# Optimization experiments

Measured on AMD Instinct MI355X. Metric: run time of the kernel, lower is better.

## Reference

```python
import jax, jax.numpy as jnp
import numpy as np

V, E, H, B, S = 50000, 256, 256, 64, 2048


def setup_inputs() -> dict:
    key = jax.random.key(0)
    ks = jax.random.split(key, 13)
    u = lambda k, shape: jax.random.uniform(k, shape, jnp.float32) - 0.5
    return {
        "inp": jax.random.randint(ks[0], (B,), 0, V, dtype=jnp.int64),
        "hidden": jax.random.normal(ks[1], (1, B, H), jnp.float32),
        "encoder_outputs": jax.random.normal(ks[2], (B, S, H), jnp.float32),
        "emb": jax.random.normal(ks[3], (V, E), jnp.float32),          # nn.Embedding weight
        "U": u(ks[4], (H, H)),
        "W": u(ks[5], (H, H)),
        "v": u(ks[6], (H, 1)),
        "W_ih": u(ks[7], (H, E)),   # RNN weight_ih_l0
        "W_hh": u(ks[8], (H, H)),   # RNN weight_hh_l0
        "b_ih": u(ks[9], (H,)),
        "b_hh": u(ks[10], (H,)),
        "W_out": u(ks[11], (V, H)),  # output Linear weight
        "b_out": u(ks[12], (V,)),
    }


def reference(inp, hidden, encoder_outputs, emb, U, W, v,
              W_ih, W_hh, b_ih, b_hh, W_out, b_out):
    # embedding lookup: (B, E)
    x = emb[inp]
    word_embs = x[:, None, :]                         # (B, 1, E)
    # Bahdanau additive attention (get_context)
    summed = jnp.tanh(word_embs @ U + encoder_outputs @ W)   # (B, S, H)
    e_ij = summed @ v                                        # (B, S, 1)
    alpha = jax.nn.softmax(e_ij, axis=1)                     # (B, S, 1)
    context = jnp.sum(alpha * encoder_outputs, axis=1)       # (B, H)
    # single tanh-RNN step; NOTE: original code feeds context as initial hidden,
    # ignoring the `hidden` argument when attention is enabled.
    h_new = jnp.tanh(x @ W_ih.T + b_ih + context @ W_hh.T + b_hh)  # (B, H)
    logits = h_new @ W_out.T + b_out                               # (B, V)
    return logits, h_new[None]                                     # hidden: (1, B, H)
```

## Files before the change

### kernel.cpp

```cpp
#include <hip/hip_runtime.h>
#include <hip/hip_bf16.h>
#include <math.h>

#define V_ 50000
#define E_ 256
#define H_ 256
#define B_ 64
#define S_ 2048
#define NCHK 32

typedef __attribute__((ext_vector_type(4))) float f32x4;
typedef __attribute__((ext_vector_type(8))) __bf16 bf16x8;

static __device__ __forceinline__ f32x4 mfma16(bf16x8 a, bf16x8 b, f32x4 c) {
  return __builtin_amdgcn_mfma_f32_16x16x32_bf16(a, b, c, 0, 0, 0);
}
static __device__ __forceinline__ float fast_tanh(float x) {
  const float e2 = __expf(2.0f * x);
  return 1.0f - 2.0f / (e2 + 1.0f);
}

__global__ __launch_bounds__(256) void prep_k(
    const int* __restrict__ inp, const float* __restrict__ emb,
    const float* __restrict__ U, const float* __restrict__ W_ih,
    const float* __restrict__ b_ih, const float* __restrict__ b_hh,
    float* __restrict__ xU, float* __restrict__ xWih) {
  const int b = blockIdx.x, h = threadIdx.x;
  __shared__ float xs[H_];
  xs[h] = emb[(size_t)inp[b] * E_ + h];
  __syncthreads();
  float au = 0.f, aw = 0.f;
  const float* __restrict__ wir = W_ih + (size_t)h * E_;
  for (int k = 0; k < H_; k += 4) {
    const float4 x4 = *reinterpret_cast<const float4*>(&xs[k]);
    const float4 w4 = *reinterpret_cast<const float4*>(wir + k);
    aw = fmaf(x4.x, w4.x, aw); aw = fmaf(x4.y, w4.y, aw);
    aw = fmaf(x4.z, w4.z, aw); aw = fmaf(x4.w, w4.w, aw);
    au = fmaf(x4.x, U[(size_t)(k + 0) * H_ + h], au);
    au = fmaf(x4.y, U[(size_t)(k + 1) * H_ + h], au);
    au = fmaf(x4.z, U[(size_t)(k + 2) * H_ + h], au);
    au = fmaf(x4.w, U[(size_t)(k + 3) * H_ + h], au);
  }
  xU[b * H_ + h] = au;
  xWih[b * H_ + h] = aw + b_ih[h] + b_hh[h];
}

__global__ __launch_bounds__(256) void prep_w(
    const float* __restrict__ W, __bf16* __restrict__ wt) {
  const int idx = blockIdx.x * 256 + threadIdx.x;
  const int n = idx >> 8, k = idx & 255;
  wt[n * H_ + (k ^ ((n & 7) << 3))] = (__bf16)W[(size_t)k * H_ + n];
}

__global__ __launch_bounds__(512) void attn_fused(
    const float* __restrict__ enc, const __bf16* __restrict__ wt,
    const float* __restrict__ xU, const float* __restrict__ vv,
    float* __restrict__ ctxp, float* __restrict__ mlout) {
  const int bx = blockIdx.x, b = blockIdx.y;
  const int t = threadIdx.x;
  const int w = t >> 6, l = t & 63, l15 = l & 15, lg = l >> 4;
  const int rg = w >> 1, cg = w & 1;

  __shared__ __bf16 Wl[H_ * H_];
  __shared__ float ered[2][128];
  __shared__ float wgt[128];
  __shared__ float mlL[2][2];

  {
    const bf16x8* __restrict__ src = reinterpret_cast<const bf16x8*>(wt);
    bf16x8* dst = reinterpret_cast<bf16x8*>(Wl);
#pragma unroll
    for (int i = 0; i < 16; ++i) dst[i * 512 + t] = src[i * 512 + t];
  }
  __syncthreads();

  for (int si = 0; si < 2; ++si) {
    const int s0 = (bx * 2 + si) * 128;
    const float* __restrict__ encS = enc + ((size_t)b * S_ + s0) * H_;
    const float* __restrict__ a0 = encS + (size_t)(rg * 32 + l15) * H_ + lg * 8;
    const float* __restrict__ a1 = encS + (size_t)(rg * 32 + 16 + l15) * H_ + lg * 8;

    f32x4 acc[2][8];
#pragma unroll
    for (int rf = 0; rf < 2; ++rf)
#pragma unroll
      for (int cf = 0; cf < 8; ++cf) acc[rf][cf] = (f32x4)(0.f);

    float4 af[2][2][2];
    af[0][0][0] = *reinterpret_cast<const float4*>(a0);
    af[0][0][1] = *reinterpret_cast<const float4*>(a0 + 4);
    af[0][1][0] = *reinterpret_cast<const float4*>(a1);
    af[0][1][1] = *reinterpret_cast<const float4*>(a1 + 4);

#pragma unroll
    for (int k = 0; k < 8; ++k) {
      const int cb = k & 1;
      if (k < 7) {
        af[cb ^ 1][0][0] = *reinterpret_cast<const float4*>(a0 + (k + 1) * 32);
        af[cb ^ 1][0][1] = *reinterpret_cast<const float4*>(a0 + (k + 1) * 32 + 4);
        af[cb ^ 1][1][0] = *reinterpret_cast<const float4*>(a1 + (k + 1) * 32);
        af[cb ^ 1][1][1] = *reinterpret_cast<const float4*>(a1 + (k + 1) * 32 + 4);
      }
      bf16x8 bb[8];
#pragma unroll
      for (int cf = 0; cf < 8; ++cf) {
        const int col = cg * 128 + cf * 16 + l15;
        bb[cf] = *reinterpret_cast<const bf16x8*>(
            &Wl[col * H_ + ((k * 32 + lg * 8) ^ ((col & 7) << 3))]);
      }
      bf16x8 ahi[2], alo[2];
#pragma unroll
      for (int rf = 0; rf < 2; ++rf) {
        const float xa[8] = {af[cb][rf][0].x, af[cb][rf][0].y, af[cb][rf][0].z, af[cb][rf][0].w,
                             af[cb][rf][1].x, af[cb][rf][1].y, af[cb][rf][1].z, af[cb][rf][1].w};
#pragma unroll
        for (int j = 0; j < 8; ++j) {
          const __bf16 hh = (__bf16)xa[j];
          ahi[rf][j] = hh;
          alo[rf][j] = (__bf16)(xa[j] - (float)hh);
        }
      }
#pragma unroll
      for (int rf = 0; rf < 2; ++rf)
#pragma unroll
        for (int cf = 0; cf < 8; ++cf) {
          acc[rf][cf] = mfma16(ahi[rf], bb[cf], acc[rf][cf]);
          acc[rf][cf] = mfma16(alo[rf], bb[cf], acc[rf][cf]);
        }
    }

    float part[2][4];
#pragma unroll
    for (int rf = 0; rf < 2; ++rf)
#pragma unroll
      for (int reg = 0; reg < 4; ++reg) part[rf][reg] = 0.f;
#pragma unroll
    for (int cf = 0; cf < 8; ++cf) {
      const int col = cg * 128 + cf * 16 + l15;
      const float xu = xU[b * H_ + col];
      const float vw = vv[col];
#pragma unroll
      for (int rf = 0; rf < 2; ++rf)
#pragma unroll
        for (int reg = 0; reg < 4; ++reg)
          part[rf][reg] += fast_tanh(xu + acc[rf][cf][reg]) * vw;
    }
#pragma unroll
    for (int o = 1; o < 16; o <<= 1)
#pragma unroll
      for (int rf = 0; rf < 2; ++rf)
#pragma unroll
        for (int reg = 0; reg < 4; ++reg)
          part[rf][reg] += __shfl_xor(part[rf][reg], o);
    if (l15 == 0) {
#pragma unroll
      for (int rf = 0; rf < 2; ++rf)
#pragma unroll
        for (int reg = 0; reg < 4; ++reg)
          ered[cg][rg * 32 + rf * 16 + lg * 4 + reg] = part[rf][reg];
    }
    __syncthreads();

    if (t < 128) {
      const float es = ered[0][t] + ered[1][t];
      float m = es;
#pragma unroll
      for (int o = 1; o < 64; o <<= 1) m = fmaxf(m, __shfl_xor(m, o));
      const float we = __expf(es - m);
      float ls = we;
#pragma unroll
      for (int o = 1; o < 64; o <<= 1) ls += __shfl_xor(ls, o);
      wgt[t] = we;
      if ((t & 63) == 0) { mlL[t >> 6][0] = m; mlL[t >> 6][1] = ls; }
    }
    __syncthreads();

    {
      const int c2 = t >> 8, h = t & 255;
      const float* __restrict__ ep = encS + (size_t)(c2 * 64) * H_ + h;
      float a = 0.f;
#pragma unroll 8
      for (int s = 0; s < 64; ++s) a = fmaf(wgt[c2 * 64 + s], ep[(size_t)s * H_], a);
      ctxp[((size_t)(bx * 4 + si * 2 + c2) * B_ + b) * H_ + h] = a;
    }
    if ((t & 255) == 0) {
      const int c2 = t >> 8;
      mlout[((bx * 4 + si * 2 + c2) * B_ + b) * 2 + 0] = mlL[c2][0];
      mlout[((bx * 4 + si * 2 + c2) * B_ + b) * 2 + 1] = mlL[c2][1];
    }
    __syncthreads();
  }
}

__global__ __launch_bounds__(256) void combine_hnew(
    const float* __restrict__ ctxp, const float* __restrict__ mlout,
    const float* __restrict__ xWih, const float* __restrict__ W_hh,
    float* __restrict__ out_h, __bf16* __restrict__ hn) {
  const int b = blockIdx.x, h = threadIdx.x;
  __shared__ float cs[H_];
  float M = -3.4e38f;
#pragma unroll
  for (int cc = 0; cc < NCHK; ++cc) M = fmaxf(M, mlout[(cc * B_ + b) * 2]);
  float num = 0.f, den = 0.f;
#pragma unroll
  for (int cc = 0; cc < NCHK; ++cc) {
    const float mw = __expf(mlout[(cc * B_ + b) * 2] - M);
    den = fmaf(mw, mlout[(cc * B_ + b) * 2 + 1], den);
    num = fmaf(mw, ctxp[((size_t)cc * B_ + b) * H_ + h], num);
  }
  cs[h] = num / den;
  __syncthreads();
  const float* __restrict__ wr = W_hh + (size_t)h * H_;
  float a = xWih[b * H_ + h];
  for (int k = 0; k < H_; k += 4) {
    const float4 w4 = *reinterpret_cast<const float4*>(wr + k);
    const float4 c4 = *reinterpret_cast<const float4*>(&cs[k]);
    a = fmaf(c4.x, w4.x, a); a = fmaf(c4.y, w4.y, a);
    a = fmaf(c4.z, w4.z, a); a = fmaf(c4.w, w4.w, a);
  }
  const float hv = fast_tanh(a);
  out_h[b * H_ + h] = hv;
  hn[b * H_ + h] = (__bf16)hv;
}

__global__ __launch_bounds__(256) void logits_mfma(
    const float* __restrict__ Wout, const float* __restrict__ bout,
    const __bf16* __restrict__ hn, float* __restrict__ logits) {
  const int v0 = blockIdx.x * 64;
  const int t = threadIdx.x;
  const int wv = t >> 6, l = t & 63, l15 = l & 15, lg = l >> 4;

  __shared__ __bf16 Wsub[8][64][32];

  {
    const int srow = t >> 2, sg = t & 3;
    const int wslot = (sg + (srow >> 1)) & 3;
    const int vc = (v0 + srow) < V_ ? (v0 + srow) : (V_ - 1);
    const float* __restrict__ wr = Wout + (size_t)vc * H_ + sg * 8;
#pragma unroll
    for (int ks = 0; ks < 8; ++ks) {
      const float4 f0 = *reinterpret_cast<const float4*>(wr + ks * 32);
      const float4 f1 = *reinterpret_cast<const float4*>(wr + ks * 32 + 4);
      const float xv[8] = {f0.x, f0.y, f0.z, f0.w, f1.x, f1.y, f1.z, f1.w};
      bf16x8 h8;
#pragma unroll
      for (int j = 0; j < 8; ++j) h8[j] = (__bf16)xv[j];
      *reinterpret_cast<bf16x8*>(&Wsub[ks][srow][wslot * 8]) = h8;
    }
  }
  __syncthreads();

  f32x4 acc[4];
#pragma unroll
  for (int i = 0; i < 4; ++i) acc[i] = (f32x4)(0.f);
  const int colb = wv * 16 + l15;
#pragma unroll
  for (int k = 0; k < 8; ++k) {
    const bf16x8 bfrag = *reinterpret_cast<const bf16x8*>(hn + (size_t)colb * H_ + k * 32 + lg * 8);
    bf16x8 ah[4];
#pragma unroll
    for (int rf = 0; rf < 4; ++rf) {
      const int rr = rf * 16 + l15;
      const int slot = (lg + (rr >> 1)) & 3;
      ah[rf] = *reinterpret_cast<const bf16x8*>(&Wsub[k][rr][slot * 8]);
    }
#pragma unroll
    for (int rf = 0; rf < 4; ++rf)
      acc[rf] = mfma16(ah[rf], bfrag, acc[rf]);
  }
#pragma unroll
  for (int rf = 0; rf < 4; ++rf) {
    const int v = v0 + rf * 16 + lg * 4;
    if (v < V_) {
      const float4 bo = *reinterpret_cast<const float4*>(bout + v);
      float4 o;
      o.x = acc[rf][0] + bo.x; o.y = acc[rf][1] + bo.y;
      o.z = acc[rf][2] + bo.z; o.w = acc[rf][3] + bo.w;
      *reinterpret_cast<float4*>(logits + (size_t)colb * V_ + v) = o;
    }
  }
}

extern "C" void kernel_launch(void* const* d_in, const int* in_sizes, int n_in,
                              void* d_out, int out_size, void* d_ws, size_t ws_size,
                              hipStream_t stream) {
  const int*   inp  = (const int*)  d_in[0];
  const float* enc  = (const float*)d_in[2];
  const float* emb  = (const float*)d_in[3];
  const float* U    = (const float*)d_in[4];
  const float* W    = (const float*)d_in[5];
  const float* v    = (const float*)d_in[6];
  const float* W_ih = (const float*)d_in[7];
  const float* W_hh = (const float*)d_in[8];
  const float* b_ih = (const float*)d_in[9];
  const float* b_hh = (const float*)d_in[10];
  const float* Wout = (const float*)d_in[11];
  const float* bout = (const float*)d_in[12];

  float* logits = (float*)d_out;
  float* out_h  = logits + (size_t)B_ * V_;

  float* ws    = (float*)d_ws;
  __bf16* wt   = (__bf16*)ws;
  float* xU    = ws + 32768;
  float* xWih  = xU + B_ * H_;
  float* ctxp  = xWih + B_ * H_;
  float* mlout = ctxp + (size_t)NCHK * B_ * H_;
  __bf16* hn   = (__bf16*)(mlout + NCHK * B_ * 2);

  prep_k<<<dim3(B_), dim3(256), 0, stream>>>(inp, emb, U, W_ih, b_ih, b_hh, xU, xWih);
  prep_w<<<dim3(H_ * H_ / 256), dim3(256), 0, stream>>>(W, wt);
  attn_fused<<<dim3(8, B_), dim3(512), 0, stream>>>(enc, wt, xU, v, ctxp, mlout);
  combine_hnew<<<dim3(B_), dim3(256), 0, stream>>>(ctxp, mlout, xWih, W_hh, out_h, hn);
  logits_mfma<<<dim3((V_ + 63) / 64), dim3(256), 0, stream>>>(Wout, bout, hn, logits);
}
```

Baseline: 111.0 us.

## Switch attention GEMM to 32x32x16 MFMA with k-octet W layout and 256-row units

```diff
diff --git a/kernel.cpp b/kernel.cpp
--- a/kernel.cpp
+++ b/kernel.cpp
@@ -10,10 +10,14 @@
 #define NCHK 32
 
 typedef __attribute__((ext_vector_type(4))) float f32x4;
+typedef __attribute__((ext_vector_type(16))) float f32x16;
 typedef __attribute__((ext_vector_type(8))) __bf16 bf16x8;
 
 static __device__ __forceinline__ f32x4 mfma16(bf16x8 a, bf16x8 b, f32x4 c) {
   return __builtin_amdgcn_mfma_f32_16x16x32_bf16(a, b, c, 0, 0, 0);
+}
+static __device__ __forceinline__ f32x16 mfma32(bf16x8 a, bf16x8 b, f32x16 c) {
+  return __builtin_amdgcn_mfma_f32_32x32x16_bf16(a, b, c, 0, 0, 0);
 }
 static __device__ __forceinline__ float fast_tanh(float x) {
   const float e2 = __expf(2.0f * x);
@@ -46,123 +50,111 @@
 }
 
 __global__ __launch_bounds__(256) void prep_w(
-    const float* __restrict__ W, __bf16* __restrict__ wt) {
+    const float* __restrict__ W, __bf16* __restrict__ wt2) {
   const int idx = blockIdx.x * 256 + threadIdx.x;
-  const int n = idx >> 8, k = idx & 255;
-  wt[n * H_ + (k ^ ((n & 7) << 3))] = (__bf16)W[(size_t)k * H_ + n];
-}
-
-__global__ __launch_bounds__(512) void attn_fused(
-    const float* __restrict__ enc, const __bf16* __restrict__ wt,
+  const int k = idx >> 8, col = idx & 255;
+  wt2[((size_t)(k >> 3) * 256 + col) * 8 + (k & 7)] = (__bf16)W[(size_t)k * H_ + col];
+}
+
+__global__ __launch_bounds__(512, 2) void attn_fused(
+    const float* __restrict__ enc, const __bf16* __restrict__ wt2,
     const float* __restrict__ xU, const float* __restrict__ vv,
     float* __restrict__ ctxp, float* __restrict__ mlout) {
-  const int bx = blockIdx.x, b = blockIdx.y;
   const int t = threadIdx.x;
-  const int w = t >> 6, l = t & 63, l15 = l & 15, lg = l >> 4;
-  const int rg = w >> 1, cg = w & 1;
-
-  __shared__ __bf16 Wl[H_ * H_];
-  __shared__ float ered[2][128];
-  __shared__ float wgt[128];
-  __shared__ float mlL[2][2];
+  const int w = t >> 6, l = t & 63, l31 = l & 31, h5 = l >> 5;
+
+  __shared__ __bf16 Wl[32 * 256 * 8];
+  __shared__ float ered[256];
+  __shared__ float wgt[4][64];
+  __shared__ float mlL[4][2];
 
   {
-    const bf16x8* __restrict__ src = reinterpret_cast<const bf16x8*>(wt);
+    const bf16x8* __restrict__ src = reinterpret_cast<const bf16x8*>(wt2);
     bf16x8* dst = reinterpret_cast<bf16x8*>(Wl);
 #pragma unroll
     for (int i = 0; i < 16; ++i) dst[i * 512 + t] = src[i * 512 + t];
   }
+  float xu[8], vw[8];
   __syncthreads();
 
-  for (int si = 0; si < 2; ++si) {
-    const int s0 = (bx * 2 + si) * 128;
-    const float* __restrict__ encS = enc + ((size_t)b * S_ + s0) * H_;
-    const float* __restrict__ a0 = encS + (size_t)(rg * 32 + l15) * H_ + lg * 8;
-    const float* __restrict__ a1 = encS + (size_t)(rg * 32 + 16 + l15) * H_ + lg * 8;
-
-    f32x4 acc[2][8];
-#pragma unroll
-    for (int rf = 0; rf < 2; ++rf)
-#pragma unroll
-      for (int cf = 0; cf < 8; ++cf) acc[rf][cf] = (f32x4)(0.f);
-
-    float4 af[2][2][2];
-    af[0][0][0] = *reinterpret_cast<const float4*>(a0);
-    af[0][0][1] = *reinterpret_cast<const float4*>(a0 + 4);
-    af[0][1][0] = *reinterpret_cast<const float4*>(a1);
-    af[0][1][1] = *reinterpret_cast<const float4*>(a1 + 4);
-
-#pragma unroll
-    for (int k = 0; k < 8; ++k) {
-      const int cb = k & 1;
-      if (k < 7) {
-        af[cb ^ 1][0][0] = *reinterpret_cast<const float4*>(a0 + (k + 1) * 32);
-        af[cb ^ 1][0][1] = *reinterpret_cast<const float4*>(a0 + (k + 1) * 32 + 4);
-        af[cb ^ 1][1][0] = *reinterpret_cast<const float4*>(a1 + (k + 1) * 32);
-        af[cb ^ 1][1][1] = *reinterpret_cast<const float4*>(a1 + (k + 1) * 32 + 4);
+#pragma unroll 1
+  for (int uu = 0; uu < 2; ++uu) {
+    const int unit = blockIdx.x * 2 + uu;
+    const int b = unit >> 3;
+    const int sidx = unit & 7;
+    const int s0 = sidx * 256;
+
+    const float* __restrict__ encA =
+        enc + ((size_t)b * S_ + s0 + w * 32 + l31) * H_ + h5 * 8;
+
+    f32x16 acc[8];
+#pragma unroll
+    for (int cf = 0; cf < 8; ++cf) acc[cf] = (f32x16)(0.f);
+
+    float4 af[2][2];
+    af[0][0] = *reinterpret_cast<const float4*>(encA);
+    af[0][1] = *reinterpret_cast<const float4*>(encA + 4);
+
+#pragma unroll
+    for (int ks = 0; ks < 16; ++ks) {
+      const int cb = ks & 1;
+      if (ks < 15) {
+        af[cb ^ 1][0] = *reinterpret_cast<const float4*>(encA + (ks + 1) * 16);
+        af[cb ^ 1][1] = *reinterpret_cast<const float4*>(encA + (ks + 1) * 16 + 4);
       }
       bf16x8 bb[8];
-#pragma unroll
-      for (int cf = 0; cf < 8; ++cf) {
-        const int col = cg * 128 + cf * 16 + l15;
+      const int koct = ks * 2 + h5;
+#pragma unroll
+      for (int cf = 0; cf < 8; ++cf)
         bb[cf] = *reinterpret_cast<const bf16x8*>(
-            &Wl[col * H_ + ((k * 32 + lg * 8) ^ ((col & 7) << 3))]);
-      }
-      bf16x8 ahi[2], alo[2];
-#pragma unroll
-      for (int rf = 0; rf < 2; ++rf) {
-        const float xa[8] = {af[cb][rf][0].x, af[cb][rf][0].y, af[cb][rf][0].z, af[cb][rf][0].w,
-                             af[cb][rf][1].x, af[cb][rf][1].y, af[cb][rf][1].z, af[cb][rf][1].w};
+            &Wl[((size_t)koct * 256 + cf * 32 + l31) * 8]);
+      bf16x8 ahi, alo;
+      {
+        const float xa[8] = {af[cb][0].x, af[cb][0].y, af[cb][0].z, af[cb][0].w,
+                             af[cb][1].x, af[cb][1].y, af[cb][1].z, af[cb][1].w};
 #pragma unroll
         for (int j = 0; j < 8; ++j) {
           const __bf16 hh = (__bf16)xa[j];
-          ahi[rf][j] = hh;
-          alo[rf][j] = (__bf16)(xa[j] - (float)hh);
+          ahi[j] = hh;
+          alo[j] = (__bf16)(xa[j] - (float)hh);
         }
       }
 #pragma unroll
-      for (int rf = 0; rf < 2; ++rf)
-#pragma unroll
-        for (int cf = 0; cf < 8; ++cf) {
-          acc[rf][cf] = mfma16(ahi[rf], bb[cf], acc[rf][cf]);
-          acc[rf][cf] = mfma16(alo[rf], bb[cf], acc[rf][cf]);
-        }
-    }
-
-    float part[2][4];
-#pragma unroll
-    for (int rf = 0; rf < 2; ++rf)
-#pragma unroll
-      for (int reg = 0; reg < 4; ++reg) part[rf][reg] = 0.f;
+      for (int cf = 0; cf < 8; ++cf) acc[cf] = mfma32(ahi, bb[cf], acc[cf]);
+#pragma unroll
+      for (int cf = 0; cf < 8; ++cf) acc[cf] = mfma32(alo, bb[cf], acc[cf]);
+    }
+
 #pragma unroll
     for (int cf = 0; cf < 8; ++cf) {
-      const int col = cg * 128 + cf * 16 + l15;
-      const float xu = xU[b * H_ + col];
-      const float vw = vv[col];
-#pragma unroll
-      for (int rf = 0; rf < 2; ++rf)
-#pragma unroll
-        for (int reg = 0; reg < 4; ++reg)
-          part[rf][reg] += fast_tanh(xu + acc[rf][cf][reg]) * vw;
-    }
-#pragma unroll
-    for (int o = 1; o < 16; o <<= 1)
-#pragma unroll
-      for (int rf = 0; rf < 2; ++rf)
-#pragma unroll
-        for (int reg = 0; reg < 4; ++reg)
-          part[rf][reg] += __shfl_xor(part[rf][reg], o);
-    if (l15 == 0) {
-#pragma unroll
-      for (int rf = 0; rf < 2; ++rf)
-#pragma unroll
-        for (int reg = 0; reg < 4; ++reg)
-          ered[cg][rg * 32 + rf * 16 + lg * 4 + reg] = part[rf][reg];
+      const int col = cf * 32 + l31;
+      xu[cf] = xU[b * H_ + col];
+      vw[cf] = vv[col];
+    }
+    float rs[16];
+#pragma unroll
+    for (int reg = 0; reg < 16; ++reg) {
+      float s = 0.f;
+#pragma unroll
+      for (int cf = 0; cf < 8; ++cf)
+        s += fast_tanh(xu[cf] + acc[cf][reg]) * vw[cf];
+      rs[reg] = s;
+    }
+#pragma unroll
+    for (int o = 1; o < 32; o <<= 1)
+#pragma unroll
+      for (int reg = 0; reg < 16; ++reg)
+        rs[reg] += __shfl_xor(rs[reg], o);
+    if (l31 == 0) {
+#pragma unroll
+      for (int reg = 0; reg < 16; ++reg)
+        ered[w * 32 + (reg & 3) + 8 * (reg >> 2) + 4 * h5] = rs[reg];
     }
     __syncthreads();
 
-    if (t < 128) {
-      const float es = ered[0][t] + ered[1][t];
+    if (t < 256) {
+      const int cidx = t >> 6, rr = t & 63;
+      const float es = ered[cidx * 64 + rr];
       float m = es;
 #pragma unroll
       for (int o = 1; o < 64; o <<= 1) m = fmaxf(m, __shfl_xor(m, o));
@@ -170,23 +162,24 @@
       float ls = we;
 #pragma unroll
       for (int o = 1; o < 64; o <<= 1) ls += __shfl_xor(ls, o);
-      wgt[t] = we;
-      if ((t & 63) == 0) { mlL[t >> 6][0] = m; mlL[t >> 6][1] = ls; }
+      wgt[cidx][rr] = we;
+      if (rr == 0) { mlL[cidx][0] = m; mlL[cidx][1] = ls; }
     }
     __syncthreads();
 
-    {
-      const int c2 = t >> 8, h = t & 255;
-      const float* __restrict__ ep = encS + (size_t)(c2 * 64) * H_ + h;
+#pragma unroll
+    for (int it = 0; it < 2; ++it) {
+      const int cc = (t >> 8) + it * 2;
+      const int h = t & 255;
+      const float* __restrict__ ep = enc + ((size_t)b * S_ + s0 + cc * 64) * H_ + h;
       float a = 0.f;
 #pragma unroll 8
-      for (int s = 0; s < 64; ++s) a = fmaf(wgt[c2 * 64 + s], ep[(size_t)s * H_], a);
-      ctxp[((size_t)(bx * 4 + si * 2 + c2) * B_ + b) * H_ + h] = a;
-    }
-    if ((t & 255) == 0) {
-      const int c2 = t >> 8;
-      mlout[((bx * 4 + si * 2 + c2) * B_ + b) * 2 + 0] = mlL[c2][0];
-      mlout[((bx * 4 + si * 2 + c2) * B_ + b) * 2 + 1] = mlL[c2][1];
+      for (int s = 0; s < 64; ++s) a = fmaf(wgt[cc][s], ep[(size_t)s * H_], a);
+      ctxp[((size_t)(sidx * 4 + cc) * B_ + b) * H_ + h] = a;
+    }
+    if (t < 8) {
+      const int cc = t >> 1;
+      mlout[((sidx * 4 + cc) * B_ + b) * 2 + (t & 1)] = mlL[cc][t & 1];
     }
     __syncthreads();
   }
@@ -301,7 +294,7 @@
   float* out_h  = logits + (size_t)B_ * V_;
 
   float* ws    = (float*)d_ws;
-  __bf16* wt   = (__bf16*)ws;
+  __bf16* wt2  = (__bf16*)ws;
   float* xU    = ws + 32768;
   float* xWih  = xU + B_ * H_;
   float* ctxp  = xWih + B_ * H_;
@@ -309,8 +302,8 @@
   __bf16* hn   = (__bf16*)(mlout + NCHK * B_ * 2);
 
   prep_k<<<dim3(B_), dim3(256), 0, stream>>>(inp, emb, U, W_ih, b_ih, b_hh, xU, xWih);
-  prep_w<<<dim3(H_ * H_ / 256), dim3(256), 0, stream>>>(W, wt);
-  attn_fused<<<dim3(8, B_), dim3(512), 0, stream>>>(enc, wt, xU, v, ctxp, mlout);
+  prep_w<<<dim3(H_ * H_ / 256), dim3(256), 0, stream>>>(W, wt2);
+  attn_fused<<<dim3(256), dim3(512), 0, stream>>>(enc, wt2, xU, v, ctxp, mlout);
   combine_hnew<<<dim3(B_), dim3(256), 0, stream>>>(ctxp, mlout, xWih, W_hh, out_h, hn);
   logits_mfma<<<dim3((V_ + 63) / 64), dim3(256), 0, stream>>>(Wout, bout, hn, logits);
 }
```

New measurement: 110.9 us. Within noise of the previous version (-0.1%).
